# Performance work log

Measured on AMD Instinct MI355X. Metric: run time of the kernel, lower is better.

Reference implementation:

```python
import jax, jax.numpy as jnp
import numpy as np

H = 32        # num query heads
HKV = 8       # num kv heads
D = 128       # head_dim
SCALE = D ** -0.5
FP8_MAX = 448.0   # e4m3 max
EPS = 1e-8
PAGE = 256
NPAGES = 20
SQ = 1024     # new diffusion tokens
CTX = 3072    # cached context tokens
DIFF_BLK = 32 # diffusion block size


def setup_inputs() -> dict:
    key = jax.random.key(0)
    ks = jax.random.split(key, 6)
    q = jax.random.normal(ks[0], (SQ, H * D), dtype=jnp.float32)
    k = jax.random.normal(ks[1], (SQ, HKV * D), dtype=jnp.float32)
    v = jax.random.normal(ks[2], (SQ, HKV * D), dtype=jnp.float32)
    # paged caches (values already stored in quantized units)
    k_cache = jax.random.normal(ks[3], (NPAGES, PAGE, HKV, D), dtype=jnp.float32)
    v_cache = jax.random.normal(ks[4], (NPAGES, PAGE, HKV, D), dtype=jnp.float32)
    # new tokens go into slots right after the context
    slot_mapping = jnp.arange(CTX, CTX + SQ, dtype=jnp.int32)
    cache_slots = jnp.arange(CTX, dtype=jnp.int32)
    # diffusion mask: full visibility of context, block-causal among new tokens
    blk = jnp.arange(SQ) // DIFF_BLK
    ctx_mask = jnp.ones((SQ, CTX), dtype=bool)
    new_mask = blk[:, None] >= blk[None, :]
    block_mask = jnp.concatenate([ctx_mask, new_mask], axis=1)  # [SQ, CTX+SQ]
    return {"q": q, "k": k, "v": v, "k_cache": k_cache, "v_cache": v_cache,
            "slot_mapping": slot_mapping, "cache_slots": cache_slots,
            "block_mask": block_mask}


def reference(q, k, v, k_cache, v_cache, slot_mapping, cache_slots, block_mask):
    k3 = k.reshape(-1, HKV, D)
    v3 = v.reshape(-1, HKV, D)
    qh = q.reshape(-1, H, D)

    # ---- FP8 scale tracking: per-kv-head absmax over (token, dim) ----
    k_scale = jnp.maximum(jnp.max(jnp.abs(k3), axis=(0, 2)) / FP8_MAX, EPS)  # [HKV]
    v_scale = jnp.maximum(jnp.max(jnp.abs(v3), axis=(0, 2)) / FP8_MAX, EPS)

    # ---- paged KV-cache store with inline quantization ----
    kc = k_cache.reshape(-1, HKV, D)  # [NPAGES*PAGE, HKV, D]
    vc = v_cache.reshape(-1, HKV, D)
    k_q = jnp.clip(k3 / k_scale[None, :, None], -FP8_MAX, FP8_MAX)
    v_q = jnp.clip(v3 / v_scale[None, :, None], -FP8_MAX, FP8_MAX)
    kc = kc.at[slot_mapping].set(k_q)
    vc = vc.at[slot_mapping].set(v_q)

    # ---- load context tokens from cache and dequantize ----
    k_ctx = kc[cache_slots] * k_scale[None, :, None]  # [CTX, HKV, D]
    v_ctx = vc[cache_slots] * v_scale[None, :, None]
    k_comb = jnp.concatenate([k_ctx, k3], axis=0)  # [SKV, HKV, D]
    v_comb = jnp.concatenate([v_ctx, v3], axis=0)

    # ---- GQA flex attention with token-level block mask ----
    G = H // HKV
    k_g = jnp.repeat(k_comb, G, axis=1)  # [SKV, H, D]
    v_g = jnp.repeat(v_comb, G, axis=1)
    scores = jnp.einsum('qhd,khd->hqk', qh, k_g) * SCALE  # [H, SQ, SKV]
    scores = jnp.where(block_mask[None, :, :], scores, jnp.float32(-1e30))
    probs = jax.nn.softmax(scores, axis=-1)
    o = jnp.einsum('hqk,khd->qhd', probs, v_g)  # [SQ, H, D]
    return o.reshape(-1, H * D)
```

## Files before the change

### kernel.cpp

```cpp
#include <hip/hip_runtime.h>
#include <stdint.h>

#define H 32
#define HKV 8
#define D 128
#define SQ 1024
#define CTX 3072
#define SKV 4096
#define FP8_MAX_C 448.0f
#define EPS_C 1e-8f

typedef __attribute__((ext_vector_type(4))) float f32x4;
typedef __attribute__((ext_vector_type(8))) __bf16 bf16x8;
typedef __attribute__((ext_vector_type(8))) unsigned short u16x8;

__device__ __forceinline__ unsigned short f2bf(float x) {
  unsigned int u = __builtin_bit_cast(unsigned int, x);
  u += 0x7fffu + ((u >> 16) & 1u);
  return (unsigned short)(u >> 16);
}

__device__ __forceinline__ f32x4 mfma16(bf16x8 a, bf16x8 b, f32x4 c) {
  return __builtin_amdgcn_mfma_f32_16x16x32_bf16(a, b, c, 0, 0, 0);
}

__device__ __forceinline__ void gld16(const unsigned short* g, char* l) {
  __builtin_amdgcn_global_load_lds(
      (const __attribute__((address_space(1))) unsigned int*)g,
      (__attribute__((address_space(3))) unsigned int*)l, 16, 0, 0);
}

__device__ __forceinline__ void stage_sync() {
  asm volatile("s_waitcnt vmcnt(0)" ::: "memory");
  __builtin_amdgcn_sched_barrier(0);
  __syncthreads();
}

__global__ void scales_part(const float* __restrict__ k,
                            const float* __restrict__ v,
                            unsigned int* __restrict__ smax) {
  const int b = blockIdx.x & 15;
  const int part = blockIdx.x >> 4;
  const float* src = (b < HKV) ? k : v;
  const int h = b & 7;
  const int tid = threadIdx.x;
  const int d0 = (tid & 31) * 4;
  float mx = 0.f;
  const int t1 = part * 128 + 128;
  for (int t = part * 128 + (tid >> 5); t < t1; t += 8) {
    float4 vv = *reinterpret_cast<const float4*>(src + (size_t)t * (HKV * D) + h * D + d0);
    mx = fmaxf(mx, fmaxf(fmaxf(fabsf(vv.x), fabsf(vv.y)),
                         fmaxf(fabsf(vv.z), fabsf(vv.w))));
  }
  __shared__ float red[256];
  red[tid] = mx;
  __syncthreads();
  for (int s = 128; s > 0; s >>= 1) {
    if (tid < s) red[tid] = fmaxf(red[tid], red[tid + s]);
    __syncthreads();
  }
  if (tid == 0) atomicMax(&smax[b], __float_as_uint(red[0]));
}

__global__ void scales_fin(const unsigned int* __restrict__ smax,
                           float* __restrict__ scales) {
  const int i = threadIdx.x;
  if (i < 16) scales[i] = fmaxf(__uint_as_float(smax[i]) / FP8_MAX_C, EPS_C);
}

__global__ void prep_kv(const float* __restrict__ k,
                        const float* __restrict__ v,
                        const float* __restrict__ k_cache,
                        const float* __restrict__ v_cache,
                        const int* __restrict__ cache_slots,
                        const float* __restrict__ scales,
                        unsigned short* __restrict__ k_comb,
                        unsigned short* __restrict__ v_combT) {
  if (blockIdx.x < 2048) {
    const int tid = blockIdx.x * 256 + threadIdx.x;
    const int d8 = tid & 15;
    const int t = (tid >> 4) & (SKV - 1);
    const int h = tid >> 16;
    const int d0 = d8 * 8;
    const float* src;
    float mul;
    if (t < CTX) {
      int slot = cache_slots[t];
      src = k_cache + (size_t)slot * (HKV * D) + h * D + d0;
      mul = scales[h];
    } else {
      src = k + (size_t)(t - CTX) * (HKV * D) + h * D + d0;
      mul = 1.f;
    }
    float4 a = *reinterpret_cast<const float4*>(src);
    float4 bb = *reinterpret_cast<const float4*>(src + 4);
    u16x8 r;
    r[0] = f2bf(a.x * mul);  r[1] = f2bf(a.y * mul);
    r[2] = f2bf(a.z * mul);  r[3] = f2bf(a.w * mul);
    r[4] = f2bf(bb.x * mul); r[5] = f2bf(bb.y * mul);
    r[6] = f2bf(bb.z * mul); r[7] = f2bf(bb.w * mul);
    *reinterpret_cast<u16x8*>(k_comb + ((size_t)h * SKV + t) * D + d0) = r;
  } else {
    const int tid = (blockIdx.x - 2048) * 256 + threadIdx.x;
    const int d = tid & 127;
    const int t8 = (tid >> 7) & 511;
    const int h = tid >> 16;
    const int t0 = t8 * 8;
    const float sc = scales[8 + h];
    u16x8 r;
#pragma unroll
    for (int i = 0; i < 8; ++i) {
      int t = t0 + i;
      float val;
      if (t < CTX) {
        int slot = cache_slots[t];
        val = v_cache[(size_t)slot * (HKV * D) + h * D + d] * sc;
      } else {
        val = v[(size_t)(t - CTX) * (HKV * D) + h * D + d];
      }
      r[i] = f2bf(val);
    }
    *reinterpret_cast<u16x8*>(v_combT + ((size_t)h * D + d) * SKV + t0) = r;
  }
}

#define LDBF(p) (*reinterpret_cast<const bf16x8*>(p))
#define Z4 ((f32x4){0.f, 0.f, 0.f, 0.f})

#define EXP4(SREG, P, RSV)                                                     \
  {                                                                            \
    P[0] = __builtin_amdgcn_exp2f(SREG[0] - m);                                \
    P[1] = __builtin_amdgcn_exp2f(SREG[1] - m);                                \
    P[2] = __builtin_amdgcn_exp2f(SREG[2] - m);                                \
    P[3] = __builtin_amdgcn_exp2f(SREG[3] - m);                                \
    RSV += (P[0] + P[1]) + (P[2] + P[3]);                                      \
  }

#define CVTPK(DST, LO, HI)                                                     \
  asm("v_cvt_pk_bf16_f32 %0, %1, %2" : "=v"(DST) : "v"(LO), "v"(HI));
#define SW32(A, B)                                                             \
  asm("v_permlane32_swap_b32 %0, %1" : "+v"(A), "+v"(B));
#define SW16(A, B)                                                             \
  asm("v_permlane16_swap_b32 %0, %1" : "+v"(A), "+v"(B));

#define PTRANS32(P0, P1, PF)                                                   \
  {                                                                            \
    unsigned int A_, Ap_, B_, Bp_;                                             \
    CVTPK(A_, P0[0], P0[1]) CVTPK(Ap_, P0[2], P0[3])                           \
    CVTPK(B_, P1[0], P1[1]) CVTPK(Bp_, P1[2], P1[3])                           \
    SW32(A_, B_) SW16(A_, B_)                                                  \
    SW32(Ap_, Bp_) SW16(Ap_, Bp_)                                              \
    union { unsigned int d[4]; bf16x8 v; } u_;                                 \
    u_.d[0] = A_; u_.d[1] = Ap_; u_.d[2] = B_; u_.d[3] = Bp_;                  \
    PF = u_.v;                                                                 \
  }

#define QKSF(SF, SA, SB)                                                       \
  {                                                                            \
    bf16x8 a0 = LDBF(kc + SF * 4096 + kx0);                                    \
    bf16x8 a1 = LDBF(kc + SF * 4096 + kx1);                                    \
    bf16x8 a2 = LDBF(kc + SF * 4096 + kx2);                                    \
    bf16x8 a3 = LDBF(kc + SF * 4096 + kx3);                                    \
    SA = mfma16(a0, qa0, SA); SA = mfma16(a1, qa1, SA);                        \
    SA = mfma16(a2, qa2, SA); SA = mfma16(a3, qa3, SA);                        \
    SB = mfma16(a0, qb0, SB); SB = mfma16(a1, qb1, SB);                        \
    SB = mfma16(a2, qb2, SB); SB = mfma16(a3, qb3, SB);                        \
  }

#define QLOADS                                                                 \
  {                                                                            \
    const float qs = 0.088388347648318447f * 1.4426950408889634f;              \
    const float* qpA = q + (size_t)(qbase + lo) * (H * D) + hqa * D;           \
    const float* qpB = qpA + D;                                                \
    _Pragma("unroll")                                                          \
    for (int ks = 0; ks < 4; ++ks) {                                           \
      float4 a = *reinterpret_cast<const float4*>(qpA + ks * 32 + g * 8);      \
      float4 b = *reinterpret_cast<const float4*>(qpA + ks * 32 + g * 8 + 4);  \
      union { unsigned short u[8]; bf16x8 v; } f;                              \
      f.u[0] = f2bf(a.x * qs); f.u[1] = f2bf(a.y * qs);                        \
      f.u[2] = f2bf(a.z * qs); f.u[3] = f2bf(a.w * qs);                        \
      f.u[4] = f2bf(b.x * qs); f.u[5] = f2bf(b.y * qs);                        \
      f.u[6] = f2bf(b.z * qs); f.u[7] = f2bf(b.w * qs);                        \
      if (ks == 0) qa0 = f.v; else if (ks == 1) qa1 = f.v;                     \
      else if (ks == 2) qa2 = f.v; else qa3 = f.v;                             \
      a = *reinterpret_cast<const float4*>(qpB + ks * 32 + g * 8);             \
      b = *reinterpret_cast<const float4*>(qpB + ks * 32 + g * 8 + 4);         \
      f.u[0] = f2bf(a.x * qs); f.u[1] = f2bf(a.y * qs);                        \
      f.u[2] = f2bf(a.z * qs); f.u[3] = f2bf(a.w * qs);                        \
      f.u[4] = f2bf(b.x * qs); f.u[5] = f2bf(b.y * qs);                        \
      f.u[6] = f2bf(b.z * qs); f.u[7] = f2bf(b.w * qs);                        \
      if (ks == 0) qb0 = f.v; else if (ks == 1) qb1 = f.v;                     \
      else if (ks == 2) qb2 = f.v; else qb3 = f.v;                             \
    }                                                                          \
  }

#define EPILOGUE(DSTEXPR)                                                      \
  lsa += __shfl_xor(lsa, 16); lsa += __shfl_xor(lsa, 32);                      \
  lsb += __shfl_xor(lsb, 16); lsb += __shfl_xor(lsb, 32);                      \
  float* dst = (DSTEXPR);                                                      \
  if (g == 0) {                                                                \
    float2 v;                                                                  \
    v.x = m; v.y = lsa;                                                        \
    *reinterpret_cast<float2*>(ml + ((size_t)part * SQ * H + (qbase + lo) * H + hqa) * 2) = v; \
    v.y = lsb;                                                                 \
    *reinterpret_cast<float2*>(ml + ((size_t)part * SQ * H + (qbase + lo) * H + hqa + 1) * 2) = v; \
  }                                                                            \
  _Pragma("unroll")                                                            \
  for (int r = 0; r < 4; ++r) {                                                \
    float* opa = dst + (size_t)(qbase + g * 4 + r) * (H * D) + hqa * D + lo;   \
    float* opb = opa + D;                                                      \
    opa[0 * 16] = aa0[r]; opb[0 * 16] = ab0[r];                                \
    opa[1 * 16] = aa1[r]; opb[1 * 16] = ab1[r];                                \
    opa[2 * 16] = aa2[r]; opb[2 * 16] = ab2[r];                                \
    opa[3 * 16] = aa3[r]; opb[3 * 16] = ab3[r];                                \
    opa[4 * 16] = aa4[r]; opb[4 * 16] = ab4[r];                                \
    opa[5 * 16] = aa5[r]; opb[5 * 16] = ab5[r];                                \
    opa[6 * 16] = aa6[r]; opb[6 * 16] = ab6[r];                                \
    opa[7 * 16] = aa7[r]; opb[7 * 16] = ab7[r];                                \
  }

#define RESCALE_ALL                                                            \
  if (!__all(pmax - m <= 8.f)) {                                               \
    float rm = fmaxf(pmax, __shfl_xor(pmax, 16));                              \
    rm = fmaxf(rm, __shfl_xor(rm, 32));                                        \
    float mn = fmaxf(m, rm);                                                   \
    float scl = __builtin_amdgcn_exp2f(m - mn);                                \
    lsa *= scl; lsb *= scl;                                                    \
    aa0 *= scl; aa1 *= scl; aa2 *= scl; aa3 *= scl;                            \
    aa4 *= scl; aa5 *= scl; aa6 *= scl; aa7 *= scl;                            \
    ab0 *= scl; ab1 *= scl; ab2 *= scl; ab3 *= scl;                            \
    ab4 *= scl; ab5 *= scl; ab6 *= scl; ab7 *= scl;                            \
    m = mn;                                                                    \
  }

#define STAGE128(TB, BUFO)                                                     \
  {                                                                            \
    _Pragma("unroll")                                                          \
    for (int j = 0; j < 4; ++j) {                                              \
      const int c = j * 128 + tid;                                             \
      const int r_ = c >> 4;                                                   \
      const int lc_ = (c & 15) ^ (r_ & 7);                                     \
      gld16(kb + (size_t)((TB) + r_) * D + lc_ * 8,                            \
            smem + (BUFO) + c * 16);                                           \
      const int dv_ = c >> 2;                                                  \
      const int cv_ = (c & 3) ^ ((dv_ >> 1) & 3);                              \
      gld16(vb + (size_t)dv_ * SKV + (TB) + cv_ * 8,                           \
            smem + (BUFO) + 8192 + c * 16);                                    \
    }                                                                          \
  }

#define PVDT32(DT, AA, AB)                                                     \
  {                                                                            \
    bf16x8 va = LDBF(vc + DT * 1024 + vx);                                     \
    AA = mfma16(pfa, va, AA);                                                  \
    AB = mfma16(pfb, va, AB);                                                  \
  }

__launch_bounds__(128, 2)
__global__ void attn_kernel(const float* __restrict__ q,
                            const unsigned short* __restrict__ k_comb,
                            const unsigned short* __restrict__ v_combT,
                            float* __restrict__ out,
                            float* __restrict__ parts,
                            float* __restrict__ ml) {
  extern __shared__ __align__(16) char smem[];
  const int bid = blockIdx.x;
  const int hkv = bid & 7;
  const int rest = bid >> 3;
  const int qs_raw = rest & 63;
  const int part = rest >> 6;
  const int qs = part ? (63 - qs_raw) : qs_raw;
  const int tid = threadIdx.x;
  const int wid = tid >> 6;
  const int l = tid & 63;
  const int lo = l & 15;
  const int g = l >> 4;
  const int qbase = qs * 16;
  const int hqa = hkv * 4 + wid * 2;
  const int n32 = 97 + (qs >> 1);
  const int t0 = (part * n32) >> 1;
  const int t1 = ((part + 1) * n32) >> 1;

  const unsigned short* kb = k_comb + (size_t)hkv * SKV * D;
  const unsigned short* vb = v_combT + (size_t)hkv * D * SKV;

  bf16x8 qa0, qa1, qa2, qa3, qb0, qb1, qb2, qb3;
  QLOADS

  f32x4 aa0 = Z4, aa1 = Z4, aa2 = Z4, aa3 = Z4;
  f32x4 aa4 = Z4, aa5 = Z4, aa6 = Z4, aa7 = Z4;
  f32x4 ab0 = Z4, ab1 = Z4, ab2 = Z4, ab3 = Z4;
  f32x4 ab4 = Z4, ab5 = Z4, ab6 = Z4, ab7 = Z4;
  float m = -1e30f;
  float lsa = 0.f, lsb = 0.f;

  const int xr = lo & 7;
  const int kx0 = ((0 + g) ^ xr) << 4;
  const int kx1 = ((4 + g) ^ xr) << 4;
  const int kx2 = ((8 + g) ^ xr) << 4;
  const int kx3 = ((12 + g) ^ xr) << 4;
  const int vx = ((g ^ ((lo >> 1) & 3))) << 4;
  const char* kbl = smem + lo * 256;
  const char* vbl = smem + 8192 + lo * 64;

  int cur = 0;
  STAGE128(t0 * 32, 0)
  stage_sync();

  for (int t = t0; t < t1; ++t) {
    if (t + 1 < t1) STAGE128((t + 1) * 32, (cur ^ 1) * 16384)

    const char* kc = kbl + cur * 16384;
    const char* vc = vbl + cur * 16384;

    f32x4 sa0 = Z4, sa1 = Z4, sb0 = Z4, sb1 = Z4;
    __builtin_amdgcn_s_setprio(1);
    QKSF(0, sa0, sb0)
    QKSF(1, sa1, sb1)
    __builtin_amdgcn_s_setprio(0);

    float pmax = fmaxf(fmaxf(fmaxf(sa0[0], sa0[1]), fmaxf(sa0[2], sa0[3])),
                       fmaxf(fmaxf(sa1[0], sa1[1]), fmaxf(sa1[2], sa1[3])));
    pmax = fmaxf(pmax,
                 fmaxf(fmaxf(fmaxf(sb0[0], sb0[1]), fmaxf(sb0[2], sb0[3])),
                       fmaxf(fmaxf(sb1[0], sb1[1]), fmaxf(sb1[2], sb1[3]))));
    RESCALE_ALL

    float pa0[4], pa1[4], pb0[4], pb1[4];
    EXP4(sa0, pa0, lsa) EXP4(sa1, pa1, lsa)
    EXP4(sb0, pb0, lsb) EXP4(sb1, pb1, lsb)

    bf16x8 pfa, pfb;
    PTRANS32(pa0, pa1, pfa)
    PTRANS32(pb0, pb1, pfb)

    __builtin_amdgcn_s_setprio(1);
    PVDT32(0, aa0, ab0)
    PVDT32(1, aa1, ab1)
    PVDT32(2, aa2, ab2)
    PVDT32(3, aa3, ab3)
    PVDT32(4, aa4, ab4)
    PVDT32(5, aa5, ab5)
    PVDT32(6, aa6, ab6)
    PVDT32(7, aa7, ab7)
    __builtin_amdgcn_s_setprio(0);

    stage_sync();
    cur ^= 1;
  }

  EPILOGUE(part == 0 ? out : parts)
}

__global__ void merge_kernel(float* __restrict__ out,
                             const float* __restrict__ parts,
                             const float* __restrict__ ml) {
  const int idx = blockIdx.x * 256 + threadIdx.x;
  const int h = (idx >> 5) & 31;
  const int qrow = idx >> 10;
  const float2* mp = (const float2*)ml;
  float2 A = mp[qrow * H + h];
  float2 B = mp[SQ * H + qrow * H + h];
  float mm = fmaxf(A.x, B.x);
  float wa = __builtin_amdgcn_exp2f(A.x - mm);
  float wb = __builtin_amdgcn_exp2f(B.x - mm);
  float inv = 1.f / (A.y * wa + B.y * wb);
  float4 oa = reinterpret_cast<float4*>(out)[idx];
  float4 ob = reinterpret_cast<const float4*>(parts)[idx];
  float4 r;
  r.x = (oa.x * wa + ob.x * wb) * inv;
  r.y = (oa.y * wa + ob.y * wb) * inv;
  r.z = (oa.z * wa + ob.z * wb) * inv;
  r.w = (oa.w * wa + ob.w * wb) * inv;
  reinterpret_cast<float4*>(out)[idx] = r;
}

extern "C" void kernel_launch(void* const* d_in, const int* in_sizes, int n_in,
                              void* d_out, int out_size, void* d_ws, size_t ws_size,
                              hipStream_t stream) {
  (void)in_sizes; (void)n_in; (void)out_size; (void)ws_size;
  const float* q = (const float*)d_in[0];
  const float* k = (const float*)d_in[1];
  const float* v = (const float*)d_in[2];
  const float* k_cache = (const float*)d_in[3];
  const float* v_cache = (const float*)d_in[4];
  const int* cache_slots = (const int*)d_in[6];
  float* out = (float*)d_out;

  unsigned int* smax = (unsigned int*)d_ws;
  float* scales = (float*)((char*)d_ws + 64);
  unsigned short* k_comb = (unsigned short*)((char*)d_ws + 256);
  unsigned short* v_combT = k_comb + (size_t)HKV * SKV * D;
  float* parts = (float*)((char*)d_ws + 256 + (size_t)16 * 1024 * 1024);
  float* ml = parts + (size_t)SQ * H * D;

  hipMemsetAsync(smax, 0, 64, stream);
  scales_part<<<128, 256, 0, stream>>>(k, v, smax);
  scales_fin<<<1, 64, 0, stream>>>(smax, scales);
  prep_kv<<<4096, 256, 0, stream>>>(k, v, k_cache, v_cache, cache_slots,
                                    scales, k_comb, v_combT);
  attn_kernel<<<1024, 128, 32768, stream>>>(q, k_comb, v_combT, out, parts, ml);
  merge_kernel<<<4096, 256, 0, stream>>>(out, parts, ml);
}
```

Baseline: 135.7 us.

## Widen attention blocks to 32 query rows and software-pipeline PV behind next QK

Each block now runs four waves covering two 16-row query slices that share the same staged K/V tiles. This halves the grid and the K/V staging traffic per query row. The loop is also software-pipelined: V fragments and the bf16 probabilities for the current tile are held in registers, so the PV MFMAs of one step run alongside the QK MFMAs of the next. The cost is higher register pressure from holding eight V fragments plus the previous probabilities, and a coarser work split across blocks.

```diff
diff --git a/kernel.cpp b/kernel.cpp
--- a/kernel.cpp
+++ b/kernel.cpp
@@ -233,11 +233,11 @@
     m = mn;                                                                    \
   }
 
-#define STAGE128(TB, BUFO)                                                     \
+#define STAGE32(TB, BUFO)                                                      \
   {                                                                            \
     _Pragma("unroll")                                                          \
-    for (int j = 0; j < 4; ++j) {                                              \
-      const int c = j * 128 + tid;                                             \
+    for (int j = 0; j < 2; ++j) {                                              \
+      const int c = j * 256 + tid;                                             \
       const int r_ = c >> 4;                                                   \
       const int lc_ = (c & 15) ^ (r_ & 7);                                     \
       gld16(kb + (size_t)((TB) + r_) * D + lc_ * 8,                            \
@@ -249,14 +249,36 @@
     }                                                                          \
   }
 
-#define PVDT32(DT, AA, AB)                                                     \
-  {                                                                            \
-    bf16x8 va = LDBF(vc + DT * 1024 + vx);                                     \
-    AA = mfma16(pfa, va, AA);                                                  \
-    AB = mfma16(pfb, va, AB);                                                  \
-  }
-
-__launch_bounds__(128, 2)
+#define SOFTMAX32                                                              \
+  float pmax = fmaxf(fmaxf(fmaxf(sa0[0], sa0[1]), fmaxf(sa0[2], sa0[3])),      \
+                     fmaxf(fmaxf(sa1[0], sa1[1]), fmaxf(sa1[2], sa1[3])));     \
+  pmax = fmaxf(pmax,                                                           \
+               fmaxf(fmaxf(fmaxf(sb0[0], sb0[1]), fmaxf(sb0[2], sb0[3])),      \
+                     fmaxf(fmaxf(sb1[0], sb1[1]), fmaxf(sb1[2], sb1[3]))));    \
+  RESCALE_ALL                                                                  \
+  float pa0[4], pa1[4], pb0[4], pb1[4];                                        \
+  EXP4(sa0, pa0, lsa) EXP4(sa1, pa1, lsa)                                      \
+  EXP4(sb0, pb0, lsb) EXP4(sb1, pb1, lsb)                                      \
+  PTRANS32(pa0, pa1, pfa)                                                      \
+  PTRANS32(pb0, pb1, pfb)
+
+#define VLOAD                                                                  \
+  vf0 = LDBF(vc + 0 * 1024 + vx); vf1 = LDBF(vc + 1 * 1024 + vx);              \
+  vf2 = LDBF(vc + 2 * 1024 + vx); vf3 = LDBF(vc + 3 * 1024 + vx);              \
+  vf4 = LDBF(vc + 4 * 1024 + vx); vf5 = LDBF(vc + 5 * 1024 + vx);              \
+  vf6 = LDBF(vc + 6 * 1024 + vx); vf7 = LDBF(vc + 7 * 1024 + vx);
+
+#define PVREG                                                                  \
+  aa0 = mfma16(pfa_p, vf0, aa0); ab0 = mfma16(pfb_p, vf0, ab0);                \
+  aa1 = mfma16(pfa_p, vf1, aa1); ab1 = mfma16(pfb_p, vf1, ab1);                \
+  aa2 = mfma16(pfa_p, vf2, aa2); ab2 = mfma16(pfb_p, vf2, ab2);                \
+  aa3 = mfma16(pfa_p, vf3, aa3); ab3 = mfma16(pfb_p, vf3, ab3);                \
+  aa4 = mfma16(pfa_p, vf4, aa4); ab4 = mfma16(pfb_p, vf4, ab4);                \
+  aa5 = mfma16(pfa_p, vf5, aa5); ab5 = mfma16(pfb_p, vf5, ab5);                \
+  aa6 = mfma16(pfa_p, vf6, aa6); ab6 = mfma16(pfb_p, vf6, ab6);                \
+  aa7 = mfma16(pfa_p, vf7, aa7); ab7 = mfma16(pfb_p, vf7, ab7);
+
+__launch_bounds__(256, 2)
 __global__ void attn_kernel(const float* __restrict__ q,
                             const unsigned short* __restrict__ k_comb,
                             const unsigned short* __restrict__ v_combT,
@@ -266,18 +288,17 @@
   extern __shared__ __align__(16) char smem[];
   const int bid = blockIdx.x;
   const int hkv = bid & 7;
-  const int rest = bid >> 3;
-  const int qs_raw = rest & 63;
-  const int part = rest >> 6;
-  const int qs = part ? (63 - qs_raw) : qs_raw;
+  const int qp_raw = (bid >> 3) & 31;
+  const int part = bid >> 8;
+  const int qp = part ? (31 - qp_raw) : qp_raw;
   const int tid = threadIdx.x;
   const int wid = tid >> 6;
   const int l = tid & 63;
   const int lo = l & 15;
   const int g = l >> 4;
-  const int qbase = qs * 16;
-  const int hqa = hkv * 4 + wid * 2;
-  const int n32 = 97 + (qs >> 1);
+  const int qbase = qp * 32 + (wid >> 1) * 16;
+  const int hqa = hkv * 4 + (wid & 1) * 2;
+  const int n32 = 97 + qp;
   const int t0 = (part * n32) >> 1;
   const int t1 = ((part + 1) * n32) >> 1;
 
@@ -303,51 +324,53 @@
   const char* kbl = smem + lo * 256;
   const char* vbl = smem + 8192 + lo * 64;
 
+  bf16x8 pfa_p, pfb_p;
+  bf16x8 vf0, vf1, vf2, vf3, vf4, vf5, vf6, vf7;
+
   int cur = 0;
-  STAGE128(t0 * 32, 0)
+  STAGE32(t0 * 32, 0)
   stage_sync();
 
-  for (int t = t0; t < t1; ++t) {
-    if (t + 1 < t1) STAGE128((t + 1) * 32, (cur ^ 1) * 16384)
-
-    const char* kc = kbl + cur * 16384;
-    const char* vc = vbl + cur * 16384;
-
+  {
+    if (t0 + 1 < t1) STAGE32((t0 + 1) * 32, 16384)
+    const char* kc = kbl;
+    const char* vc = vbl;
     f32x4 sa0 = Z4, sa1 = Z4, sb0 = Z4, sb1 = Z4;
     __builtin_amdgcn_s_setprio(1);
     QKSF(0, sa0, sb0)
     QKSF(1, sa1, sb1)
     __builtin_amdgcn_s_setprio(0);
-
-    float pmax = fmaxf(fmaxf(fmaxf(sa0[0], sa0[1]), fmaxf(sa0[2], sa0[3])),
-                       fmaxf(fmaxf(sa1[0], sa1[1]), fmaxf(sa1[2], sa1[3])));
-    pmax = fmaxf(pmax,
-                 fmaxf(fmaxf(fmaxf(sb0[0], sb0[1]), fmaxf(sb0[2], sb0[3])),
-                       fmaxf(fmaxf(sb1[0], sb1[1]), fmaxf(sb1[2], sb1[3]))));
-    RESCALE_ALL
-
-    float pa0[4], pa1[4], pb0[4], pb1[4];
-    EXP4(sa0, pa0, lsa) EXP4(sa1, pa1, lsa)
-    EXP4(sb0, pb0, lsb) EXP4(sb1, pb1, lsb)
-
     bf16x8 pfa, pfb;
-    PTRANS32(pa0, pa1, pfa)
-    PTRANS32(pb0, pb1, pfb)
-
+    SOFTMAX32
+    VLOAD
+    pfa_p = pfa; pfb_p = pfb;
+    stage_sync();
+    cur = 1;
+  }
+
+  for (int t = t0 + 1; t < t1; ++t) {
+    if (t + 1 < t1) STAGE32((t + 1) * 32, (cur ^ 1) * 16384)
+
+    const char* kc = kbl + cur * 16384;
+    const char* vc = vbl + cur * 16384;
+
+    f32x4 sa0 = Z4, sa1 = Z4, sb0 = Z4, sb1 = Z4;
     __builtin_amdgcn_s_setprio(1);
-    PVDT32(0, aa0, ab0)
-    PVDT32(1, aa1, ab1)
-    PVDT32(2, aa2, ab2)
-    PVDT32(3, aa3, ab3)
-    PVDT32(4, aa4, ab4)
-    PVDT32(5, aa5, ab5)
-    PVDT32(6, aa6, ab6)
-    PVDT32(7, aa7, ab7)
+    QKSF(0, sa0, sb0)
+    QKSF(1, sa1, sb1)
+    PVREG
     __builtin_amdgcn_s_setprio(0);
+
+    bf16x8 pfa, pfb;
+    SOFTMAX32
+    VLOAD
+    pfa_p = pfa; pfb_p = pfb;
 
     stage_sync();
     cur ^= 1;
   }
+
+  PVREG
 
   EPILOGUE(part == 0 ? out : parts)
 }
@@ -399,6 +422,6 @@
   scales_fin<<<1, 64, 0, stream>>>(smax, scales);
   prep_kv<<<4096, 256, 0, stream>>>(k, v, k_cache, v_cache, cache_slots,
                                     scales, k_comb, v_combT);
-  attn_kernel<<<1024, 128, 32768, stream>>>(q, k_comb, v_combT, out, parts, ml);
+  attn_kernel<<<512, 256, 32768, stream>>>(q, k_comb, v_combT, out, parts, ml);
   merge_kernel<<<4096, 256, 0, stream>>>(out, parts, ml);
 }
```

After: 110.9 us. -18.3%, faster.
